# Kernel tuning notes

Hardware: AMD Instinct MI355X
Metric: run time of the kernel (lower is better)

Reference implementation:

```python
import jax, jax.numpy as jnp
import numpy as np

LEAK = 0.2
N, C, T, H, DOUT = 512, 16, 15, 32, 32


def setup_inputs() -> dict:
    key = jax.random.key(0)
    k = jax.random.split(key, 5)
    x = jax.random.normal(k[0], (N, C), dtype=jnp.float32)
    adj = jax.random.uniform(k[1], (N, N, T), dtype=jnp.float32)
    W1 = jax.random.normal(k[2], (2 * C, T + 1, H), dtype=jnp.float32) * 0.05
    W2 = jax.random.normal(k[3], (2 * C, T + 1, DOUT), dtype=jnp.float32) * 0.05
    W3 = jax.random.normal(k[4], (C, H), dtype=jnp.float32) * 0.05
    return {"x": x, "adj": adj, "W1": W1, "W2": W2, "W3": W3}


def reference(x, adj, W1, W2, W3):
    n, c = x.shape
    # input_diag: [N,N,C,1], diagonal copy of node features
    diag = jnp.einsum('mn,ni->mni', jnp.eye(n, dtype=x.dtype), x)[..., None]
    # D = concat(adj-weighted broadcast of x, diag) along edge-type axis -> [N,N,C,T+1]
    D = jnp.concatenate([jnp.einsum('mnt,ni->mnit', adj, x), diag], axis=3)
    # symmetrize along channel axis -> [N,N,2C,T+1]
    D = jnp.concatenate([D, jnp.transpose(D, (1, 0, 2, 3))], axis=2)
    K = jnp.einsum('mnit,ith->mnh', D, W1)   # [N,N,H]
    V = jnp.einsum('mnit,itd->mnd', D, W2)   # [N,N,DOUT]
    Q = x @ W3                               # [N,H]
    logits1 = jnp.einsum('nh,nmh->nm', Q, K)
    logits2 = jnp.einsum('mh,nmh->nm', Q, K)
    s1 = jax.nn.softmax(logits1, axis=1)
    s2 = jax.nn.softmax(logits2, axis=0)
    temp = jnp.einsum('nm,nmd->nd', s1, V) + jnp.einsum('nm,nmd->md', s2, V)
    return jnp.maximum(temp, LEAK * temp)  # lrelu
```

## Files before the change

kernel.cpp:

```cpp
#include <hip/hip_runtime.h>
#include <hip/hip_bf16.h>

#define NNODE 512
#define CCH   16
#define TT    15
#define TP    16
#define HH    32
#define DD    32

typedef unsigned short u16;
typedef unsigned int   u32;
typedef short bf8 __attribute__((ext_vector_type(8)));
typedef float f4  __attribute__((ext_vector_type(4)));

__device__ __forceinline__ float bf2f(u16 v) {
    union { u32 u; float f; } x; x.u = ((u32)v) << 16; return x.f;
}
__device__ __forceinline__ u16 f2bf(float f) {
    union { float f; u32 u; } x; x.f = f;
    u32 u = x.u;
    return (u16)((u + 0x7FFFu + ((u >> 16) & 1u)) >> 16);
}
__device__ __forceinline__ void unpack8(uint4 p, float* o) {
    o[0]=bf2f((u16)(p.x & 0xffffu)); o[1]=bf2f((u16)(p.x >> 16));
    o[2]=bf2f((u16)(p.y & 0xffffu)); o[3]=bf2f((u16)(p.y >> 16));
    o[4]=bf2f((u16)(p.z & 0xffffu)); o[5]=bf2f((u16)(p.z >> 16));
    o[6]=bf2f((u16)(p.w & 0xffffu)); o[7]=bf2f((u16)(p.w >> 16));
}
__device__ __forceinline__ uint4 pack8(const u16* v) {
    return make_uint4((u32)v[0]|((u32)v[1]<<16), (u32)v[2]|((u32)v[3]<<16),
                      (u32)v[4]|((u32)v[5]<<16), (u32)v[6]|((u32)v[7]<<16));
}

__global__ __launch_bounds__(256) void k_prep_adjp(
    const float* __restrict__ x, const float* __restrict__ W1,
    const float* __restrict__ W2, const float* __restrict__ W3,
    const float* __restrict__ adj,
    u16* __restrict__ A1, u16* __restrict__ B1,
    u16* __restrict__ A2T, u16* __restrict__ B2T,
    u16* __restrict__ Qb, float* __restrict__ QAd, float* __restrict__ QB,
    u16* __restrict__ adjP, u16* __restrict__ adjPT)
{
    int tid = threadIdx.x;
    if (blockIdx.x < 512) {
        int n = blockIdx.x;
        __shared__ alignas(16) float xs[CCH];
        __shared__ alignas(16) float A1row[512], B1row[512];
        __shared__ alignas(16) float A2row[512], B2row[512];
        __shared__ alignas(16) float Qs[HH];
        if (tid < CCH) xs[tid] = x[n*CCH + tid];
        __syncthreads();
        float xr[CCH];
        #pragma unroll
        for (int i=0;i<CCH;i++) xr[i]=xs[i];
        #pragma unroll
        for (int rep=0; rep<2; rep++) {
            int c = tid + rep*256;
            float a1=0.f,b1=0.f,a2=0.f,b2=0.f;
            #pragma unroll
            for (int i=0;i<CCH;i++) {
                a1 += xr[i]*W1[i*512 + c];
                b1 += xr[i]*W1[(CCH+i)*512 + c];
                a2 += xr[i]*W2[i*512 + c];
                b2 += xr[i]*W2[(CCH+i)*512 + c];
            }
            A1[(size_t)n*512 + c]=f2bf(a1); B1[(size_t)n*512 + c]=f2bf(b1);
            A1row[c]=a1; B1row[c]=b1; A2row[c]=a2; B2row[c]=b2;
        }
        if (tid < HH) {
            float q=0.f;
            #pragma unroll
            for (int i=0;i<CCH;i++) q += xr[i]*W3[i*HH + tid];
            Qs[tid]=q; Qb[(size_t)n*HH + tid]=f2bf(q);
        }
        __syncthreads();
        if (tid < TP) {
            float qa=0.f, qb=0.f;
            #pragma unroll
            for (int h=0;h<HH;h++) { qa += Qs[h]*A1row[tid*HH+h]; qb += Qs[h]*B1row[tid*HH+h]; }
            QAd[(size_t)n*TP + tid]=qa; QB[(size_t)n*TP + tid]=qb;
        }
        {
            int d = tid >> 3, t0 = (tid & 7) * 2;
            u32 pa = (u32)f2bf(A2row[t0*32 + d]) | ((u32)f2bf(A2row[(t0+1)*32 + d]) << 16);
            u32 pb = (u32)f2bf(B2row[t0*32 + d]) | ((u32)f2bf(B2row[(t0+1)*32 + d]) << 16);
            *(u32*)(A2T + (size_t)d*8192 + n*16 + t0) = pa;
            *(u32*)(B2T + (size_t)d*8192 + n*16 + t0) = pb;
        }
    } else {
        int b = blockIdx.x - 512;
        int n0 = (b >> 4) * 32, m0 = (b & 15) * 32;
        __shared__ alignas(16) u16 s[32*520];
        #pragma unroll
        for (int i = 0; i < 60; i++) {
            int e = tid + i*256;
            int nl = e / 480; int rem = e - nl*480;
            int ml = rem / 15; int t = rem - ml*15;
            float v = adj[((size_t)(n0+nl)*512 + (m0+ml))*TT + t];
            s[nl*520 + ml*16 + t] = f2bf(v);
        }
        #pragma unroll
        for (int i = 0; i < 4; i++) {
            int e = tid + i*256; int nl = e >> 5, ml = e & 31;
            s[nl*520 + ml*16 + 15] = ((n0+nl) == (m0+ml)) ? (u16)0x3F80 : (u16)0;
        }
        __syncthreads();
        #pragma unroll
        for (int i = 0; i < 8; i++) {
            int c = tid + i*256;
            int nl = c >> 6, off = (c & 63) * 8;
            uint4 vv = *(const uint4*)(s + nl*520 + off);
            *(uint4*)(adjP + (size_t)(n0+nl)*8192 + m0*16 + off) = vv;
        }
        #pragma unroll
        for (int i = 0; i < 8; i++) {
            int c = tid + i*256;
            int ml = c >> 6, nlh = c & 63, nl = nlh >> 1, half = nlh & 1;
            uint4 vv = *(const uint4*)(s + nl*520 + ml*16 + half*8);
            *(uint4*)(adjPT + (size_t)(m0+ml)*8192 + (n0+nl)*16 + half*8) = vv;
        }
    }
}

__global__ __launch_bounds__(256) void k_logits(
    const u16* __restrict__ Qb, const u16* __restrict__ A1, const u16* __restrict__ B1,
    const u16* __restrict__ adjP, const u16* __restrict__ adjPT,
    const float* __restrict__ QAd, const float* __restrict__ QB,
    float* __restrict__ L1, float* __restrict__ L2T)
{
    const int m0 = blockIdx.x * 16, n0 = blockIdx.y * 16;
    const int tid = threadIdx.x;
    const int wv = tid >> 6, lane = tid & 63, l15 = lane & 15, quad = lane >> 4;
    __shared__ alignas(16) float sL1[16*17];
    __shared__ alignas(16) float sL2[16*17];

    bf8 afragN = *(const bf8*)(Qb + (size_t)(n0 + l15)*32 + quad*8);
    bf8 afragM = *(const bf8*)(Qb + (size_t)(m0 + l15)*32 + quad*8);

    f4 accG[4], accH[4];
    #pragma unroll
    for (int j = 0; j < 4; j++) {
        int m = m0 + wv*4 + j;
        int n = n0 + wv*4 + j;
        bf8 bG = *(const bf8*)(A1 + (size_t)m*512 + l15*32 + quad*8);
        bf8 bH = *(const bf8*)(B1 + (size_t)n*512 + l15*32 + quad*8);
        f4 z = {0.f,0.f,0.f,0.f};
        accG[j] = __builtin_amdgcn_mfma_f32_16x16x32_bf16(afragN, bG, z, 0, 0, 0);
        accH[j] = __builtin_amdgcn_mfma_f32_16x16x32_bf16(afragM, bH, z, 0, 0, 0);
    }

    #pragma unroll
    for (int j = 0; j < 4; j++) {
        int m = m0 + wv*4 + j;
        #pragma unroll
        for (int r = 0; r < 4; r++) {
            int n = n0 + quad*4 + r;
            float a  = bf2f(adjP [(size_t)n*8192 + m*16 + l15]);
            float at = bf2f(adjPT[(size_t)n*8192 + m*16 + l15]);
            float v = a*accG[j][r] + at*QB[n*16 + l15];
            #pragma unroll
            for (int o = 1; o < 16; o <<= 1) v += __shfl_xor(v, o, 64);
            if (l15 == 0) sL1[(quad*4+r)*17 + wv*4 + j] = v;
        }
    }
    #pragma unroll
    for (int j = 0; j < 4; j++) {
        int n = n0 + wv*4 + j;
        #pragma unroll
        for (int r = 0; r < 4; r++) {
            int m = m0 + quad*4 + r;
            float a  = bf2f(adjP [(size_t)n*8192 + m*16 + l15]);
            float at = bf2f(adjPT[(size_t)n*8192 + m*16 + l15]);
            float v = a*QAd[m*16 + l15] + at*accH[j][r];
            #pragma unroll
            for (int o = 1; o < 16; o <<= 1) v += __shfl_xor(v, o, 64);
            if (l15 == 0) sL2[(quad*4+r)*17 + wv*4 + j] = v;
        }
    }
    __syncthreads();
    int row = tid >> 4, col = tid & 15;
    L1 [(size_t)(n0+row)*NNODE + m0 + col] = sL1[row*17+col];
    L2T[(size_t)(m0+row)*NNODE + n0 + col] = sL2[row*17+col];
}

__global__ __launch_bounds__(256) void k_softmax_w(
    const float* __restrict__ L1, const float* __restrict__ L2T,
    const u16* __restrict__ adjP, const u16* __restrict__ adjPT,
    u16* __restrict__ W1c, u16* __restrict__ W2c,
    float* __restrict__ u1, float* __restrict__ v2)
{
    int b = blockIdx.x, tid = threadIdx.x;
    bool first = b < NNODE;
    int j = first ? b : b - NNODE;
    const float* row = first ? (L1 + (size_t)j*NNODE) : (L2T + (size_t)j*NNODE);
    u16* W  = (first ? W1c : W2c) + (size_t)j*8192;
    float* uv = (first ? u1 : v2) + (size_t)j*TP;

    float v0 = row[tid], v1 = row[tid+256];
    float mx = fmaxf(v0, v1);
    #pragma unroll
    for (int o=32; o; o>>=1) mx = fmaxf(mx, __shfl_xor(mx, o, 64));
    __shared__ alignas(16) float red[4], red2[4], ur[4][16];
    int lane = tid & 63, wv = tid >> 6;
    if (!lane) red[wv] = mx;
    __syncthreads();
    mx = fmaxf(fmaxf(red[0],red[1]), fmaxf(red[2],red[3]));
    float e0 = __expf(v0 - mx), e1 = __expf(v1 - mx);
    float sm = e0 + e1;
    #pragma unroll
    for (int o=32; o; o>>=1) sm += __shfl_xor(sm, o, 64);
    if (!lane) red2[wv] = sm;
    __syncthreads();
    float inv = 1.0f / (red2[0]+red2[1]+red2[2]+red2[3]);
    float sa = e0*inv, sb = e1*inv;

    const u16* ap = adjP  + (size_t)j*8192;
    const u16* tp = adjPT + (size_t)j*8192;
    float u[16];
    #pragma unroll
    for (int t=0;t<16;t++) u[t]=0.f;
    #pragma unroll
    for (int half = 0; half < 2; half++) {
        int k = tid + half*256;
        float sv = half ? sb : sa;
        const uint4* p = (const uint4*)(ap + k*16);
        float av[16]; unpack8(p[0], av); unpack8(p[1], av+8);
        u16 o16[16];
        #pragma unroll
        for (int t=0;t<16;t++) o16[t] = f2bf(sv*av[t]);
        uint4* wp = (uint4*)(W + k*16);
        wp[0] = pack8(o16); wp[1] = pack8(o16+8);
        const uint4* q = (const uint4*)(tp + k*16);
        float tv[16]; unpack8(q[0], tv); unpack8(q[1], tv+8);
        #pragma unroll
        for (int t=0;t<16;t++) u[t] = fmaf(sv, tv[t], u[t]);
    }
    #pragma unroll
    for (int t=0;t<16;t++) {
        #pragma unroll
        for (int o=32; o; o>>=1) u[t] += __shfl_xor(u[t], o, 64);
    }
    if (!lane) {
        #pragma unroll
        for (int t=0;t<16;t++) ur[wv][t] = u[t];
    }
    __syncthreads();
    if (tid < 16) uv[tid] = ur[0][tid]+ur[1][tid]+ur[2][tid]+ur[3][tid];
}

__global__ __launch_bounds__(256) void k_gemm2(
    const u16* __restrict__ W1c, const u16* __restrict__ W2c,
    const u16* __restrict__ A2T, const u16* __restrict__ B2T,
    float* __restrict__ tempP)
{
    int tid = threadIdx.x;
    int wv = tid >> 6, lane = tid & 63, l15 = lane & 15, quad = lane >> 4;
    int w = blockIdx.x*4 + wv;
    int kc = w & 15, dt = (w >> 4) & 1, jt = w >> 5;
    size_t aRow = (size_t)(jt*16 + l15)*8192;
    size_t bRow = (size_t)(dt*16 + l15)*8192;
    int kt0 = kc*512 + quad*8;
    f4 acc = {0.f, 0.f, 0.f, 0.f};
    #pragma unroll
    for (int s = 0; s < 16; s++) {
        int kt = kt0 + s*32;
        bf8 aw1 = *(const bf8*)(W1c + aRow + kt);
        bf8 ba2 = *(const bf8*)(A2T + bRow + kt);
        acc = __builtin_amdgcn_mfma_f32_16x16x32_bf16(aw1, ba2, acc, 0, 0, 0);
        bf8 aw2 = *(const bf8*)(W2c + aRow + kt);
        bf8 bb2 = *(const bf8*)(B2T + bRow + kt);
        acc = __builtin_amdgcn_mfma_f32_16x16x32_bf16(aw2, bb2, acc, 0, 0, 0);
    }
    #pragma unroll
    for (int r = 0; r < 4; r++)
        tempP[((size_t)kc*NNODE + jt*16 + quad*4 + r)*DD + dt*16 + l15] = acc[r];
}

__global__ __launch_bounds__(256) void k_final(
    const float* __restrict__ tempP, const float* __restrict__ u1, const float* __restrict__ v2,
    const u16* __restrict__ A2T, const u16* __restrict__ B2T, float* __restrict__ out)
{
    int base = blockIdx.x * 256 + threadIdx.x;
    int j = base >> 5, d = base & 31;
    float acc = 0.f;
    #pragma unroll
    for (int kc=0;kc<16;kc++) acc += tempP[((size_t)kc*NNODE + j)*DD + d];
    const uint4* pb2 = (const uint4*)(B2T + (size_t)d*8192 + j*16);
    const uint4* pa2 = (const uint4*)(A2T + (size_t)d*8192 + j*16);
    float bv[16], av[16];
    unpack8(pb2[0], bv); unpack8(pb2[1], bv+8);
    unpack8(pa2[0], av); unpack8(pa2[1], av+8);
    #pragma unroll
    for (int t = 0; t < 16; t++)
        acc += u1[(size_t)j*TP + t]*bv[t] + v2[(size_t)j*TP + t]*av[t];
    out[(size_t)j*DD + d] = fmaxf(acc, 0.2f*acc);
}

extern "C" void kernel_launch(void* const* d_in, const int* in_sizes, int n_in,
                              void* d_out, int out_size, void* d_ws, size_t ws_size,
                              hipStream_t stream)
{
    (void)in_sizes; (void)n_in; (void)out_size; (void)ws_size;
    const float* x   = (const float*)d_in[0];
    const float* adj = (const float*)d_in[1];
    const float* W1  = (const float*)d_in[2];
    const float* W2  = (const float*)d_in[3];
    const float* W3  = (const float*)d_in[4];

    char* ws = (char*)d_ws;
    u16*   adjP = (u16*)(ws);
    u16*   adjPT= (u16*)(ws + 0x800000);
    u16*   W1c  = (u16*)(ws + 0x1000000);
    u16*   W2c  = (u16*)(ws + 0x1800000);
    u16*   A1   = (u16*)(ws + 0x2000000);
    u16*   B1   = (u16*)(ws + 0x2080000);
    u16*   A2T  = (u16*)(ws + 0x2100000);
    u16*   B2T  = (u16*)(ws + 0x2180000);
    u16*   Qb   = (u16*)(ws + 0x2200000);
    float* QAd  = (float*)(ws + 0x2210000);
    float* QB   = (float*)(ws + 0x2220000);
    float* u1   = (float*)(ws + 0x2230000);
    float* v2   = (float*)(ws + 0x2240000);
    float* L1   = (float*)(ws + 0x2300000);
    float* L2T  = (float*)(ws + 0x2400000);
    float* tempP= (float*)(ws + 0x2500000);

    k_prep_adjp<<<768, 256, 0, stream>>>(x, W1, W2, W3, adj,
                                         A1, B1, A2T, B2T, Qb, QAd, QB, adjP, adjPT);
    k_logits<<<dim3(32,32), 256, 0, stream>>>(Qb, A1, B1, adjP, adjPT, QAd, QB, L1, L2T);
    k_softmax_w<<<1024, 256, 0, stream>>>(L1, L2T, adjP, adjPT, W1c, W2c, u1, v2);
    k_gemm2<<<256, 256, 0, stream>>>(W1c, W2c, A2T, B2T, tempP);
    k_final<<<64, 256, 0, stream>>>(tempP, u1, v2, A2T, B2T, (float*)d_out);
}
```

Before: 116.3 us.

## Swap MFMA operands in logits and use butterfly transpose-reduction in softmax

The logits kernel swaps the MFMA operands so each lane holds four consecutive edge-type results. The adjacency weighting then becomes a per-lane dot product using vectorized uint2 loads and two cross-quad shuffles, replacing 16 scattered scalar loads and 4-step shuffle reductions per output. The softmax kernel replaces 16 independent 6-step wave reductions with a recursive-halving butterfly that reduces all 16 accumulators in about 21 shuffles, writing results through a bit-reversed index. This cuts shuffle count and memory transactions, at the cost of more intricate index logic.

```diff
diff --git a/kernel.cpp b/kernel.cpp
--- a/kernel.cpp
+++ b/kernel.cpp
@@ -134,48 +134,52 @@
     __shared__ alignas(16) float sL1[16*17];
     __shared__ alignas(16) float sL2[16*17];
 
-    bf8 afragN = *(const bf8*)(Qb + (size_t)(n0 + l15)*32 + quad*8);
-    bf8 afragM = *(const bf8*)(Qb + (size_t)(m0 + l15)*32 + quad*8);
-
-    f4 accG[4], accH[4];
+    bf8 qbN = *(const bf8*)(Qb + (size_t)(n0 + l15)*32 + quad*8);
+    bf8 qbM = *(const bf8*)(Qb + (size_t)(m0 + l15)*32 + quad*8);
+    float4 qb4 = *(const float4*)(QB  + (size_t)(n0 + l15)*TP + quad*4);
+    float4 qa4 = *(const float4*)(QAd + (size_t)(m0 + l15)*TP + quad*4);
+
     #pragma unroll
     for (int j = 0; j < 4; j++) {
         int m = m0 + wv*4 + j;
-        int n = n0 + wv*4 + j;
-        bf8 bG = *(const bf8*)(A1 + (size_t)m*512 + l15*32 + quad*8);
-        bf8 bH = *(const bf8*)(B1 + (size_t)n*512 + l15*32 + quad*8);
+        bf8 aA1 = *(const bf8*)(A1 + (size_t)m*512 + l15*32 + quad*8);
         f4 z = {0.f,0.f,0.f,0.f};
-        accG[j] = __builtin_amdgcn_mfma_f32_16x16x32_bf16(afragN, bG, z, 0, 0, 0);
-        accH[j] = __builtin_amdgcn_mfma_f32_16x16x32_bf16(afragM, bH, z, 0, 0, 0);
-    }
-
-    #pragma unroll
-    for (int j = 0; j < 4; j++) {
-        int m = m0 + wv*4 + j;
-        #pragma unroll
-        for (int r = 0; r < 4; r++) {
-            int n = n0 + quad*4 + r;
-            float a  = bf2f(adjP [(size_t)n*8192 + m*16 + l15]);
-            float at = bf2f(adjPT[(size_t)n*8192 + m*16 + l15]);
-            float v = a*accG[j][r] + at*QB[n*16 + l15];
-            #pragma unroll
-            for (int o = 1; o < 16; o <<= 1) v += __shfl_xor(v, o, 64);
-            if (l15 == 0) sL1[(quad*4+r)*17 + wv*4 + j] = v;
-        }
+        f4 g = __builtin_amdgcn_mfma_f32_16x16x32_bf16(aA1, qbN, z, 0, 0, 0);
+        uint2 ax = *(const uint2*)(adjPT + (size_t)m*8192 + (n0 + l15)*16 + quad*4);
+        uint2 ay = *(const uint2*)(adjP  + (size_t)m*8192 + (n0 + l15)*16 + quad*4);
+        float v;
+        v = bf2f((u16)(ax.x & 0xffffu)) * g[0];
+        v = fmaf(bf2f((u16)(ax.x >> 16)),     g[1], v);
+        v = fmaf(bf2f((u16)(ax.y & 0xffffu)), g[2], v);
+        v = fmaf(bf2f((u16)(ax.y >> 16)),     g[3], v);
+        v = fmaf(bf2f((u16)(ay.x & 0xffffu)), qb4.x, v);
+        v = fmaf(bf2f((u16)(ay.x >> 16)),     qb4.y, v);
+        v = fmaf(bf2f((u16)(ay.y & 0xffffu)), qb4.z, v);
+        v = fmaf(bf2f((u16)(ay.y >> 16)),     qb4.w, v);
+        v += __shfl_xor(v, 16, 64);
+        v += __shfl_xor(v, 32, 64);
+        if (quad == 0) sL1[l15*17 + wv*4 + j] = v;
     }
     #pragma unroll
     for (int j = 0; j < 4; j++) {
         int n = n0 + wv*4 + j;
-        #pragma unroll
-        for (int r = 0; r < 4; r++) {
-            int m = m0 + quad*4 + r;
-            float a  = bf2f(adjP [(size_t)n*8192 + m*16 + l15]);
-            float at = bf2f(adjPT[(size_t)n*8192 + m*16 + l15]);
-            float v = a*QAd[m*16 + l15] + at*accH[j][r];
-            #pragma unroll
-            for (int o = 1; o < 16; o <<= 1) v += __shfl_xor(v, o, 64);
-            if (l15 == 0) sL2[(quad*4+r)*17 + wv*4 + j] = v;
-        }
+        bf8 aB1 = *(const bf8*)(B1 + (size_t)n*512 + l15*32 + quad*8);
+        f4 z = {0.f,0.f,0.f,0.f};
+        f4 h = __builtin_amdgcn_mfma_f32_16x16x32_bf16(aB1, qbM, z, 0, 0, 0);
+        uint2 ax = *(const uint2*)(adjPT + (size_t)n*8192 + (m0 + l15)*16 + quad*4);
+        uint2 ay = *(const uint2*)(adjP  + (size_t)n*8192 + (m0 + l15)*16 + quad*4);
+        float v;
+        v = bf2f((u16)(ax.x & 0xffffu)) * h[0];
+        v = fmaf(bf2f((u16)(ax.x >> 16)),     h[1], v);
+        v = fmaf(bf2f((u16)(ax.y & 0xffffu)), h[2], v);
+        v = fmaf(bf2f((u16)(ax.y >> 16)),     h[3], v);
+        v = fmaf(bf2f((u16)(ay.x & 0xffffu)), qa4.x, v);
+        v = fmaf(bf2f((u16)(ay.x >> 16)),     qa4.y, v);
+        v = fmaf(bf2f((u16)(ay.y & 0xffffu)), qa4.z, v);
+        v = fmaf(bf2f((u16)(ay.y >> 16)),     qa4.w, v);
+        v += __shfl_xor(v, 16, 64);
+        v += __shfl_xor(v, 32, 64);
+        if (quad == 0) sL2[l15*17 + wv*4 + j] = v;
     }
     __syncthreads();
     int row = tid >> 4, col = tid & 15;
@@ -236,13 +240,33 @@
         for (int t=0;t<16;t++) u[t] = fmaf(sv, tv[t], u[t]);
     }
     #pragma unroll
-    for (int t=0;t<16;t++) {
-        #pragma unroll
-        for (int o=32; o; o>>=1) u[t] += __shfl_xor(u[t], o, 64);
-    }
-    if (!lane) {
-        #pragma unroll
-        for (int t=0;t<16;t++) ur[wv][t] = u[t];
+    for (int i=0;i<8;i++) {
+        float s0 = (lane&1) ? u[i] : u[i+8];
+        float r0 = __shfl_xor(s0, 1, 64);
+        u[i] = ((lane&1) ? u[i+8] : u[i]) + r0;
+    }
+    #pragma unroll
+    for (int i=0;i<4;i++) {
+        float s0 = (lane&2) ? u[i] : u[i+4];
+        float r0 = __shfl_xor(s0, 2, 64);
+        u[i] = ((lane&2) ? u[i+4] : u[i]) + r0;
+    }
+    #pragma unroll
+    for (int i=0;i<2;i++) {
+        float s0 = (lane&4) ? u[i] : u[i+2];
+        float r0 = __shfl_xor(s0, 4, 64);
+        u[i] = ((lane&4) ? u[i+2] : u[i]) + r0;
+    }
+    {
+        float s0 = (lane&8) ? u[0] : u[1];
+        float r0 = __shfl_xor(s0, 8, 64);
+        u[0] = ((lane&8) ? u[1] : u[0]) + r0;
+    }
+    u[0] += __shfl_xor(u[0], 16, 64);
+    u[0] += __shfl_xor(u[0], 32, 64);
+    if (lane < 16) {
+        int tm = ((lane&1)<<3) | ((lane&2)<<1) | ((lane&4)>>1) | ((lane&8)>>3);
+        ur[wv][tm] = u[0];
     }
     __syncthreads();
     if (tid < 16) uv[tid] = ur[0][tid]+ur[1][tid]+ur[2][tid]+ur[3][tid];
```

Measured after the change: 106.8 us. -8.1%, faster.
